# Performance work log

Hardware: AMD Instinct MI355X
Metric: run time of the kernel (lower is better)

Reference implementation:

```python
import jax, jax.numpy as jnp
import numpy as np

B, H, S, D = 2, 16, 2048, 128

def setup_inputs() -> dict:
    key = jax.random.key(0)
    kq, kk, kv = jax.random.split(key, 3)
    Q = jax.random.normal(kq, (B, H, S, D), dtype=jnp.float32)
    K = jax.random.normal(kk, (B, H, S, D), dtype=jnp.float32)
    V = jax.random.normal(kv, (B, H, S, D), dtype=jnp.float32)
    return {"Q": Q, "K": K, "V": V}

def reference(Q, K, V):
    # FlashAttentionV3 forward: scaled dot-product attention with causal mask,
    # scale defaults to 1/sqrt(head_dim), dropout=0.
    head_dim = Q.shape[-1]
    scale = 1.0 / jnp.sqrt(jnp.asarray(head_dim, dtype=Q.dtype))
    # scores: [B, H, S, S]
    scores = jnp.einsum('bhqd,bhkd->bhqk', Q, K) * scale
    seq_q, seq_k = Q.shape[2], K.shape[2]
    causal_mask = jnp.tril(jnp.ones((seq_q, seq_k), dtype=bool))  # [S, S]
    scores = jnp.where(causal_mask, scores, jnp.asarray(-jnp.inf, dtype=scores.dtype))
    attn = jax.nn.softmax(scores, axis=-1)
    out = jnp.einsum('bhqk,bhkd->bhqd', attn, V)
    return out
```

## Files before the change

### kernel.cpp

```cpp
#include <hip/hip_runtime.h>
#include <hip/hip_bf16.h>

typedef __attribute__((ext_vector_type(8))) short short8;
typedef __attribute__((ext_vector_type(4))) float f32x4;
typedef __attribute__((ext_vector_type(4))) unsigned int u32x4;

#define S_LEN 2048
#define D_DIM 128
#define NT 32
#define NQT 16
#define TILE_FRAG_BYTES 16384u
#define VF_OFF ((size_t)32 * NT * TILE_FRAG_BYTES)

__device__ __forceinline__ unsigned short bfbits(float f) {
  return __builtin_bit_cast(unsigned short, __float2bfloat16(f));
}
__device__ __forceinline__ unsigned int pk2(float lo, float hi) {
  return (unsigned int)bfbits(lo) | ((unsigned int)bfbits(hi) << 16);
}
__device__ __forceinline__ float exp2f_hw(float x) {
  float r;
  asm("v_exp_f32 %0, %1" : "=v"(r) : "v"(x));
  return r;
}
__device__ __forceinline__ void gload16(const void* g, void* l) {
  __builtin_amdgcn_global_load_lds(
      (const __attribute__((address_space(1))) unsigned int*)g,
      (__attribute__((address_space(3))) unsigned int*)l, 16, 0, 0);
}

extern "C" __global__ void __launch_bounds__(256)
fa_prepass_kernel(const float* __restrict__ Kg, const float* __restrict__ Vg,
                  char* __restrict__ ws)
{
  const unsigned gid = blockIdx.x * 256 + threadIdx.x;
  const unsigned g = gid & ((1u << 20) - 1);
  const int ln = g & 63, l15 = ln & 15, lhi = (ln >> 4) & 3;
  const int f  = (g >> 6) & 15;
  const int t  = (g >> 10) & 31;
  const int bh = g >> 15;
  char* dst = ws + ((size_t)(bh * NT + t) * 16 + f) * 1024 + ln * 16;
  if (gid < (1u << 20)) {
    const int c = f >> 2, kk = f & 3;
    const int row = t * 64 + ((l15 >> 2) << 3) + (l15 & 3) + ((c & 1) << 2) + ((c >> 1) << 5);
    const float* src = Kg + (size_t)bh * S_LEN * D_DIM + (size_t)row * D_DIM + kk * 32 + lhi * 8;
    f32x4 a = *(const f32x4*)src;
    f32x4 b = *(const f32x4*)(src + 4);
    u32x4 u;
    u[0] = pk2(a[0], a[1]); u[1] = pk2(a[2], a[3]);
    u[2] = pk2(b[0], b[1]); u[3] = pk2(b[2], b[3]);
    *(u32x4*)dst = u;
  } else {
    const int dc = f >> 1, w = f & 1;
    const float* src = Vg + (size_t)bh * S_LEN * D_DIM
                     + (size_t)(t * 64 + w * 32 + lhi * 8) * D_DIM + dc * 16 + l15;
    float v[8];
    #pragma unroll
    for (int j = 0; j < 8; ++j) v[j] = src[(size_t)j * D_DIM];
    u32x4 u;
    u[0] = pk2(v[0], v[1]); u[1] = pk2(v[2], v[3]);
    u[2] = pk2(v[4], v[5]); u[3] = pk2(v[6], v[7]);
    *(u32x4*)(dst + VF_OFF) = u;
  }
}

extern "C" __global__ void __launch_bounds__(256, 2)
fa_fwd_kernel(const float* __restrict__ Qg, const char* __restrict__ ws,
              float* __restrict__ Og)
{
  __shared__ __align__(16) char smem[2][32768];

  const int bh = blockIdx.x;
  const int qt = (NQT - 1) - (int)blockIdx.y;
  const int m0 = qt * 128;
  const int tid = threadIdx.x;
  const int wv  = tid >> 6;
  const int ln  = tid & 63;
  const int l15 = ln & 15;
  const int lhi = ln >> 4;

  const float* Qb = Qg + (size_t)bh * S_LEN * D_DIM;
  float*       Ob = Og + (size_t)bh * S_LEN * D_DIM;
  const char*  kfb = ws + (size_t)bh * NT * TILE_FRAG_BYTES;
  const int    voff = ln * 16;

  const float scale = 0.12753102f;
  const int wrow_lo = m0 + wv * 32;

  short8 qf[2][4];
  #pragma unroll
  for (int g = 0; g < 2; ++g) {
    const float* qsrc = Qb + (size_t)(wrow_lo + g * 16 + l15) * D_DIM + lhi * 8;
    #pragma unroll
    for (int kk = 0; kk < 4; ++kk) {
      f32x4 a = *(const f32x4*)(qsrc + kk * 32);
      f32x4 b = *(const f32x4*)(qsrc + kk * 32 + 4);
      u32x4 u;
      u[0] = pk2(a[0] * scale, a[1] * scale);
      u[1] = pk2(a[2] * scale, a[3] * scale);
      u[2] = pk2(b[0] * scale, b[1] * scale);
      u[3] = pk2(b[2] * scale, b[3] * scale);
      qf[g][kk] = __builtin_bit_cast(short8, u);
    }
  }

  auto stage = [&](int t, char* buf) {
    const char* kt = kfb + (size_t)t * TILE_FRAG_BYTES;
    #pragma unroll
    for (int i = 0; i < 8; ++i) {
      const int fi = wv * 8 + i;
      const size_t src_off = (fi < 16) ? (size_t)fi * 1024
                                       : VF_OFF + (size_t)(fi - 16) * 1024;
      gload16(kt + src_off + voff, buf + fi * 1024);
    }
  };

  const f32x4 fzero = {0.f, 0.f, 0.f, 0.f};
  f32x4 oacc[2][8];
  #pragma unroll
  for (int g = 0; g < 2; ++g)
    #pragma unroll
    for (int i = 0; i < 8; ++i) oacc[g][i] = fzero;
  float m_run[2] = {8.0f, 8.0f};
  float l_run[2] = {0.f, 0.f};

  const int ntiles = 2 * qt + 2;

  stage(0, smem[0]);
  __syncthreads();

  int cur = 0;
  for (int t = 0; t < ntiles; ++t) {
    const int kv0 = t * 64;
    const bool comp = (kv0 <= wrow_lo + 31);
    if (t + 1 < ntiles) stage(t + 1, smem[cur ^ 1]);

    if (comp) {
      const char* kt = smem[cur];
      const char* vt = smem[cur] + 16 * 1024;

      f32x4 sacc[2][4];
      __builtin_amdgcn_s_setprio(1);
      #pragma unroll
      for (int c = 0; c < 4; ++c) {
        sacc[0][c] = fzero; sacc[1][c] = fzero;
        #pragma unroll
        for (int kk = 0; kk < 4; ++kk) {
          short8 kf = *(const short8*)(kt + (c * 4 + kk) * 1024 + voff);
          sacc[0][c] = __builtin_amdgcn_mfma_f32_16x16x32_bf16(kf, qf[0][kk], sacc[0][c], 0, 0, 0);
          sacc[1][c] = __builtin_amdgcn_mfma_f32_16x16x32_bf16(kf, qf[1][kk], sacc[1][c], 0, 0, 0);
        }
      }
      __builtin_amdgcn_s_setprio(0);

      if (kv0 + 63 > wrow_lo) {
        #pragma unroll
        for (int g = 0; g < 2; ++g) {
          const int qg = wrow_lo + g * 16 + l15;
          #pragma unroll
          for (int c = 0; c < 4; ++c) {
            const int kvb = kv0 + (c >> 1) * 32 + (c & 1) * 4 + lhi * 8;
            #pragma unroll
            for (int r = 0; r < 4; ++r)
              if (kvb + r > qg) sacc[g][c][r] = -INFINITY;
          }
        }
      }

      float mt[2];
      #pragma unroll
      for (int g = 0; g < 2; ++g) {
        float mA[4];
        #pragma unroll
        for (int r = 0; r < 4; ++r)
          mA[r] = fmaxf(fmaxf(sacc[g][0][r], sacc[g][1][r]),
                        fmaxf(sacc[g][2][r], sacc[g][3][r]));
        mt[g] = fmaxf(fmaxf(mA[0], mA[1]), fmaxf(mA[2], mA[3]));
        #pragma unroll
        for (int c = 0; c < 4; ++c)
          #pragma unroll
          for (int r = 0; r < 4; ++r)
            sacc[g][c][r] = exp2f_hw(sacc[g][c][r] - m_run[g]);
      }
      #pragma unroll
      for (int g = 0; g < 2; ++g) {
        float m = fmaxf(mt[g], __shfl_xor(mt[g], 16));
        m = fmaxf(m, __shfl_xor(m, 32));
        if (!__all(m <= m_run[g] + 11.5f)) {
          const float m_new = fmaxf(m_run[g], m);
          const float al = exp2f_hw(m_run[g] - m_new);
          #pragma unroll
          for (int c = 0; c < 4; ++c)
            #pragma unroll
            for (int r = 0; r < 4; ++r) sacc[g][c][r] *= al;
          #pragma unroll
          for (int dc = 0; dc < 8; ++dc)
            #pragma unroll
            for (int r = 0; r < 4; ++r) oacc[g][dc][r] *= al;
          l_run[g] *= al;
          m_run[g] = m_new;
        }
        float sA[4];
        #pragma unroll
        for (int r = 0; r < 4; ++r)
          sA[r] = (sacc[g][0][r] + sacc[g][1][r]) + (sacc[g][2][r] + sacc[g][3][r]);
        float rs = (sA[0] + sA[1]) + (sA[2] + sA[3]);
        rs += __shfl_xor(rs, 16);
        rs += __shfl_xor(rs, 32);
        l_run[g] += rs;
      }

      short8 pfrag[2][2];
      #pragma unroll
      for (int g = 0; g < 2; ++g)
        #pragma unroll
        for (int w = 0; w < 2; ++w) {
          u32x4 u;
          u[0] = pk2(sacc[g][2 * w][0], sacc[g][2 * w][1]);
          u[1] = pk2(sacc[g][2 * w][2], sacc[g][2 * w][3]);
          u[2] = pk2(sacc[g][2 * w + 1][0], sacc[g][2 * w + 1][1]);
          u[3] = pk2(sacc[g][2 * w + 1][2], sacc[g][2 * w + 1][3]);
          pfrag[g][w] = __builtin_bit_cast(short8, u);
        }

      __builtin_amdgcn_s_setprio(1);
      #pragma unroll
      for (int dc = 0; dc < 8; ++dc) {
        #pragma unroll
        for (int w = 0; w < 2; ++w) {
          short8 vf = *(const short8*)(vt + (dc * 2 + w) * 1024 + voff);
          oacc[0][dc] = __builtin_amdgcn_mfma_f32_16x16x32_bf16(vf, pfrag[0][w], oacc[0][dc], 0, 0, 0);
          oacc[1][dc] = __builtin_amdgcn_mfma_f32_16x16x32_bf16(vf, pfrag[1][w], oacc[1][dc], 0, 0, 0);
        }
      }
      __builtin_amdgcn_s_setprio(0);
    }

    __syncthreads();
    cur ^= 1;
  }

  #pragma unroll
  for (int g = 0; g < 2; ++g) {
    const float invl = 1.0f / l_run[g];
    float* orow = Ob + (size_t)(wrow_lo + g * 16 + l15) * D_DIM + lhi * 4;
    #pragma unroll
    for (int dc = 0; dc < 8; ++dc) {
      f32x4 o;
      #pragma unroll
      for (int r = 0; r < 4; ++r) o[r] = oacc[g][dc][r] * invl;
      *(f32x4*)(orow + dc * 16) = o;
    }
  }
}

extern "C" void kernel_launch(void* const* d_in, const int* in_sizes, int n_in,
                              void* d_out, int out_size, void* d_ws, size_t ws_size,
                              hipStream_t stream) {
  const float* Q = (const float*)d_in[0];
  const float* K = (const float*)d_in[1];
  const float* V = (const float*)d_in[2];
  float* O = (float*)d_out;
  char* ws = (char*)d_ws;
  fa_prepass_kernel<<<dim3(8192), dim3(256), 0, stream>>>(K, V, ws);
  dim3 grid(32 , NQT);
  fa_fwd_kernel<<<grid, dim3(256), 0, stream>>>(Q, ws, O);
}
```

Measured before the change: 88.74 us.

## Load V fragments directly from global into registers and interleave q-tile order

```diff
diff --git a/kernel.cpp b/kernel.cpp
--- a/kernel.cpp
+++ b/kernel.cpp
@@ -68,10 +68,11 @@
 fa_fwd_kernel(const float* __restrict__ Qg, const char* __restrict__ ws,
               float* __restrict__ Og)
 {
-  __shared__ __align__(16) char smem[2][32768];
+  __shared__ __align__(16) char smem[2][16384];
 
   const int bh = blockIdx.x;
-  const int qt = (NQT - 1) - (int)blockIdx.y;
+  const int by = (int)blockIdx.y;
+  const int qt = (by < 8) ? (15 - 2 * by) : (2 * (by - 8));
   const int m0 = qt * 128;
   const int tid = threadIdx.x;
   const int wv  = tid >> 6;
@@ -82,6 +83,7 @@
   const float* Qb = Qg + (size_t)bh * S_LEN * D_DIM;
   float*       Ob = Og + (size_t)bh * S_LEN * D_DIM;
   const char*  kfb = ws + (size_t)bh * NT * TILE_FRAG_BYTES;
+  const char*  vfbg = kfb + VF_OFF;
   const int    voff = ln * 16;
 
   const float scale = 0.12753102f;
@@ -104,14 +106,12 @@
     }
   }
 
-  auto stage = [&](int t, char* buf) {
+  auto stage_k = [&](int t, char* buf) {
     const char* kt = kfb + (size_t)t * TILE_FRAG_BYTES;
     #pragma unroll
-    for (int i = 0; i < 8; ++i) {
-      const int fi = wv * 8 + i;
-      const size_t src_off = (fi < 16) ? (size_t)fi * 1024
-                                       : VF_OFF + (size_t)(fi - 16) * 1024;
-      gload16(kt + src_off + voff, buf + fi * 1024);
+    for (int i = 0; i < 4; ++i) {
+      const int fi = wv * 4 + i;
+      gload16(kt + (size_t)fi * 1024 + voff, buf + fi * 1024);
     }
   };
 
@@ -126,18 +126,18 @@
 
   const int ntiles = 2 * qt + 2;
 
-  stage(0, smem[0]);
+  stage_k(0, smem[0]);
   __syncthreads();
 
   int cur = 0;
   for (int t = 0; t < ntiles; ++t) {
     const int kv0 = t * 64;
     const bool comp = (kv0 <= wrow_lo + 31);
-    if (t + 1 < ntiles) stage(t + 1, smem[cur ^ 1]);
+    if (t + 1 < ntiles) stage_k(t + 1, smem[cur ^ 1]);
 
     if (comp) {
       const char* kt = smem[cur];
-      const char* vt = smem[cur] + 16 * 1024;
+      const char* vg = vfbg + (size_t)t * TILE_FRAG_BYTES;
 
       f32x4 sacc[2][4];
       __builtin_amdgcn_s_setprio(1);
@@ -152,6 +152,11 @@
         }
       }
       __builtin_amdgcn_s_setprio(0);
+
+      short8 vfA[8];
+      #pragma unroll
+      for (int i = 0; i < 8; ++i)
+        vfA[i] = *(const short8*)(vg + i * 1024 + voff);
 
       if (kv0 + 63 > wrow_lo) {
         #pragma unroll
@@ -223,16 +228,26 @@
           pfrag[g][w] = __builtin_bit_cast(short8, u);
         }
 
+      short8 vfB[8];
+      #pragma unroll
+      for (int i = 0; i < 8; ++i)
+        vfB[i] = *(const short8*)(vg + (8 + i) * 1024 + voff);
+
       __builtin_amdgcn_s_setprio(1);
       #pragma unroll
-      for (int dc = 0; dc < 8; ++dc) {
+      for (int dc = 0; dc < 4; ++dc)
         #pragma unroll
         for (int w = 0; w < 2; ++w) {
-          short8 vf = *(const short8*)(vt + (dc * 2 + w) * 1024 + voff);
-          oacc[0][dc] = __builtin_amdgcn_mfma_f32_16x16x32_bf16(vf, pfrag[0][w], oacc[0][dc], 0, 0, 0);
-          oacc[1][dc] = __builtin_amdgcn_mfma_f32_16x16x32_bf16(vf, pfrag[1][w], oacc[1][dc], 0, 0, 0);
-        }
-      }
+          oacc[0][dc] = __builtin_amdgcn_mfma_f32_16x16x32_bf16(vfA[dc * 2 + w], pfrag[0][w], oacc[0][dc], 0, 0, 0);
+          oacc[1][dc] = __builtin_amdgcn_mfma_f32_16x16x32_bf16(vfA[dc * 2 + w], pfrag[1][w], oacc[1][dc], 0, 0, 0);
+        }
+      #pragma unroll
+      for (int dc = 4; dc < 8; ++dc)
+        #pragma unroll
+        for (int w = 0; w < 2; ++w) {
+          oacc[0][dc] = __builtin_amdgcn_mfma_f32_16x16x32_bf16(vfB[(dc - 4) * 2 + w], pfrag[0][w], oacc[0][dc], 0, 0, 0);
+          oacc[1][dc] = __builtin_amdgcn_mfma_f32_16x16x32_bf16(vfB[(dc - 4) * 2 + w], pfrag[1][w], oacc[1][dc], 0, 0, 0);
+        }
       __builtin_amdgcn_s_setprio(0);
     }
 
```

Result: faster. 86.89 us (-2.1%).
